# Kernel tuning notes

Hardware: AMD Instinct MI355X
Metric: run time of the kernel (lower is better)

## Reference

```python
import jax, jax.numpy as jnp
import numpy as np


def setup_inputs() -> dict:
    key = jax.random.key(0)
    ks = jax.random.split(key, 8)
    d, h = 1024, 256
    bl, bh = 2048, 2048
    b = bl + bh
    w = lambda k, shp: jax.random.normal(k, shp, jnp.float32) * 0.02
    return {
        "z_low": jax.random.normal(ks[0], (bl, d), jnp.float32),
        "z_high": jax.random.normal(ks[1], (bh, d), jnp.float32),
        "z_bar": jax.random.normal(ks[2], (b, d), jnp.float32),
        "z_normal": jax.random.normal(ks[3], (b, d), jnp.float32),
        "Wa1": w(ks[4], (d, h)), "ba1": jnp.zeros((h,), jnp.float32),
        "Wa2": w(ks[5], (h,)), "ba2": jnp.zeros((), jnp.float32),
        "W0": w(ks[6], (d, d)), "b0": jnp.zeros((d,), jnp.float32),
        "W1": w(ks[7], (d, d)), "b1": jnp.zeros((d,), jnp.float32),
    }


def _scores(x, Wa1, ba1, Wa2, ba2):
    # Linear -> tanh -> Linear(->1); returns per-row attention logits [N]
    return jnp.tanh(x @ Wa1 + ba1) @ Wa2 + ba2


def _integrate(x, Wa1, ba1, Wa2, ba2):
    a = jax.nn.softmax(_scores(x, Wa1, ba1, Wa2, ba2))  # [N]
    return a @ x  # [dim]


def _loo_pool(x, Wa1, ba1, Wa2, ba2):
    # batched leave-one-out attention pooling: row i pools over all j != i
    n = x.shape[0]
    s = _scores(x, Wa1, ba1, Wa2, ba2)  # [N]
    S = jnp.broadcast_to(s[None, :], (n, n))
    S = jnp.where(jnp.eye(n, dtype=bool), -jnp.inf, S)
    A = jax.nn.softmax(S, axis=-1)  # [N,N], zero on diagonal
    return A @ x  # [N, dim]


def _cos(a, b, eps=1e-8):
    na = jnp.maximum(jnp.linalg.norm(a, axis=-1), eps)
    nb = jnp.maximum(jnp.linalg.norm(b, axis=-1), eps)
    return jnp.sum(a * b, axis=-1) / (na * nb)


def reference(z_low, z_high, z_bar, z_normal, Wa1, ba1, Wa2, ba2, W0, b0, W1, b1):
    z_all = jnp.concatenate([z_low, z_high], axis=0)  # [B, d]
    batch = z_all.shape[0]

    z_hat = jnp.concatenate([
        _loo_pool(z_low, Wa1, ba1, Wa2, ba2),
        _loo_pool(z_high, Wa1, ba1, Wa2, ba2),
    ], axis=0)  # [B, d]
    z_tumor = _loo_pool(z_all, Wa1, ba1, Wa2, ba2)  # [B, d]
    z_norm = _integrate(z_normal, Wa1, ba1, Wa2, ba2)  # [d]

    lin0 = lambda v: v @ W0 + b0
    lin1 = lambda v: v @ W1 + b1

    base = lin0(z_hat) + lin1(z_bar)
    pred_tumor = base + lin0(z_tumor)          # [B, d]
    pred_normal = base + lin0(z_norm)[None, :]  # [B, d]

    cpc_tumor = z_all @ pred_tumor.T    # [B, B]
    cpc_normal = z_all @ pred_normal.T  # [B, B]
    eye = jnp.eye(batch, dtype=cpc_tumor.dtype)
    total = eye * cpc_tumor + (1.0 - eye) * cpc_normal

    loss_tcl = jnp.sum(jnp.diag(jax.nn.log_softmax(total, axis=1))) / (-1.0 * batch)

    ones = jnp.ones((batch,), z_all.dtype)
    cos_loss = jnp.mean(ones - _cos(z_all, z_hat)) + jnp.mean(ones - _cos(z_all, z_bar))
    hinge_in = _cos(z_all, pred_tumor) - _cos(z_all, pred_normal)
    hinge = jnp.mean(jnp.maximum(0.0, 1.0 - hinge_in))  # HingeEmbeddingLoss, target=-1, margin=1
    loss_adc = cos_loss + hinge

    return (loss_tcl, loss_adc)
```

## Files before the change

kernel.cpp:

```cpp
#include <hip/hip_runtime.h>
#include <math.h>

#define D     1024
#define H     256
#define BLOW  2048
#define BTOT  4096
#define NCHUNK 64

using bf16x8 = __attribute__((ext_vector_type(8))) __bf16;
using f32x4  = __attribute__((ext_vector_type(4))) float;

static const size_t OFF_ZALL = 0;
static const size_t OFF_C    = 4194304;
static const size_t OFF_PT   = 8388608;
static const size_t T0       = 12582912;
static const size_t OFF_SALL = T0;
static const size_t OFF_SNORM= T0 + 4096;
static const size_t OFF_EGRP = T0 + 8192;
static const size_t OFF_ENORM= T0 + 16384;
static const size_t OFF_PLOW = T0 + 20480;
static const size_t OFF_PHIGH= T0 + 21504;
static const size_t OFF_PNORM= T0 + 22528;
static const size_t OFF_PALL = T0 + 23552;
static const size_t OFF_ZNV  = T0 + 24576;
static const size_t OFF_WNORM= T0 + 25600;
static const size_t OFF_BIASC= T0 + 26624;
static const size_t OFF_STATS= T0 + 27648;
static const size_t OFF_ACC  = T0 + 27664;
static const size_t OFF_NZ   = T0 + 27680;
static const size_t OFF_DT   = T0 + 31776;
static const size_t OFF_G    = T0 + 35872;
static const size_t OFF_DIAG = T0 + 39968;
static const size_t OFF_PART = T0 + 44064;
static const size_t BF_BASE_F = 13160448;
static const size_t BF_ZALLN= 0;
static const size_t BF_ZHAT = 8388608;
static const size_t BF_ZTUM = 12582912;
static const size_t BF_ZBAR = 16777216;
static const size_t BF_C    = 20971520;
static const size_t BF_W0T  = 25165824;
static const size_t BF_W1T  = 26214400;
static const size_t BF_WA1T = 27262976;

__device__ inline unsigned short f2bf(float f){
  unsigned u = __float_as_uint(f);
  u += 0x7fffu + ((u >> 16) & 1u);
  return (unsigned short)(u >> 16);
}
__device__ inline float wave_sum(float v){
#pragma unroll
  for (int o = 32; o > 0; o >>= 1) v += __shfl_xor(v, o);
  return v;
}
__device__ inline float wave_maxf(float v){
#pragma unroll
  for (int o = 32; o > 0; o >>= 1) v = fmaxf(v, __shfl_xor(v, o));
  return v;
}
__device__ inline float block_sum(float v, float* sb){
  v = wave_sum(v);
  __syncthreads();
  if ((threadIdx.x & 63) == 0) sb[threadIdx.x >> 6] = v;
  __syncthreads();
  return sb[0] + sb[1] + sb[2] + sb[3];
}
__device__ inline float block_maxf(float v, float* sb){
  v = wave_maxf(v);
  __syncthreads();
  if ((threadIdx.x & 63) == 0) sb[threadIdx.x >> 6] = v;
  __syncthreads();
  return fmaxf(fmaxf(sb[0], sb[1]), fmaxf(sb[2], sb[3]));
}

__device__ inline void gload16(const unsigned short* g, unsigned short* l){
  __builtin_amdgcn_global_load_lds(
      (const __attribute__((address_space(1))) unsigned int*)g,
      (__attribute__((address_space(3))) unsigned int*)l, 16, 0, 0);
}

__global__ __launch_bounds__(256) void k_prep(const float* __restrict__ zl,
        const float* __restrict__ zh, const float* __restrict__ znorm,
        const float* __restrict__ zbar, float* __restrict__ za,
        unsigned short* __restrict__ zalln_bf, unsigned short* __restrict__ zbar_bf){
  int row = blockIdx.x, t = threadIdx.x, job = blockIdx.z;
  if (job == 0){
    const float4* src = (const float4*)((row < BLOW) ? (zl + (size_t)row * D)
                                                     : (zh + (size_t)(row - BLOW) * D));
    float4 v = src[t];
    ((float4*)(za + (size_t)row * D))[t] = v;
    *(ushort4*)(zalln_bf + (size_t)row * D + t * 4) =
        make_ushort4(f2bf(v.x), f2bf(v.y), f2bf(v.z), f2bf(v.w));
  } else if (job == 1){
    float4 v = ((const float4*)(znorm + (size_t)row * D))[t];
    *(ushort4*)(zalln_bf + (size_t)(BTOT + row) * D + t * 4) =
        make_ushort4(f2bf(v.x), f2bf(v.y), f2bf(v.z), f2bf(v.w));
  } else {
    float4 v = ((const float4*)(zbar + (size_t)row * D))[t];
    *(ushort4*)(zbar_bf + (size_t)row * D + t * 4) =
        make_ushort4(f2bf(v.x), f2bf(v.y), f2bf(v.z), f2bf(v.w));
  }
}

__global__ __launch_bounds__(256) void k_tconv3(const float* __restrict__ W0,
        const float* __restrict__ W1, const float* __restrict__ Wa1,
        unsigned short* __restrict__ W0T, unsigned short* __restrict__ W1T,
        unsigned short* __restrict__ Wa1T){
  __shared__ float tile[32][33];
  int z = blockIdx.z;
  const float* in; unsigned short* out; int R, C;
  if (z == 0){ in = W0; out = W0T; R = D; C = D; }
  else if (z == 1){ in = W1; out = W1T; R = D; C = D; }
  else { if (blockIdx.x >= 8) return; in = Wa1; out = Wa1T; R = D; C = H; }
  int t = threadIdx.x;
  int lr = t >> 3;
  int lc = (t & 7) << 2;
  int gr = blockIdx.y * 32, gc = blockIdx.x * 32;
  float4 v = *(const float4*)(in + (size_t)(gr + lr) * C + gc + lc);
  tile[lr][lc + 0] = v.x; tile[lr][lc + 1] = v.y; tile[lr][lc + 2] = v.z; tile[lr][lc + 3] = v.w;
  __syncthreads();
  ushort4 o = make_ushort4(f2bf(tile[lc + 0][lr]), f2bf(tile[lc + 1][lr]),
                           f2bf(tile[lc + 2][lr]), f2bf(tile[lc + 3][lr]));
  *(ushort4*)(out + (size_t)(gc + lr) * R + gr + lc) = o;
}

__global__ __launch_bounds__(256) void k_zero13(float* __restrict__ ws){
  int i = blockIdx.x * 256 + threadIdx.x;
  if (i < 8192) ws[OFF_SALL + i] = 0.f;
  else if (i < 12288) ws[OFF_PLOW + i - 8192] = 0.f;
  else if (i < 13312) ws[OFF_WNORM + i - 12288] = 0.f;
  else if (i < 13328) ws[OFF_ACC + i - 13312] = 0.f;
}

__device__ inline void mfma_core_db(const unsigned short* __restrict__ A,
                                    const unsigned short* __restrict__ B,
                                    int row0, int col0,
                                    unsigned short* lds,
                                    f32x4 acc[4][4]){
  int t = threadIdx.x;
  int l = t & 63, w = t >> 6;
  int wrow = w >> 1, wcol = w & 1;
  int g = l >> 4, c15 = l & 15;
  const unsigned short* a0 = A + (size_t)(row0 + (t >> 2)) * 1024 + ((t & 3) << 3);
  const unsigned short* a1 = a0 + (size_t)64 * 1024;
  const unsigned short* b0 = B + (size_t)(col0 + (t >> 2)) * 1024 + ((t & 3) << 3);
  const unsigned short* b1 = b0 + (size_t)64 * 1024;
  int sd = w * 512;
  int abase = (wrow * 64 + c15) * 32 + g * 8;
  int bbase = 4096 + (wcol * 64 + c15) * 32 + g * 8;
  unsigned short* buf = lds;
  unsigned short* nxt = lds + 8192;
  gload16(a0, buf + sd);
  gload16(a1, buf + 2048 + sd);
  gload16(b0, buf + 4096 + sd);
  gload16(b1, buf + 6144 + sd);
  __syncthreads();
  for (int kb = 0; kb < 1024; kb += 32){
    if (kb + 32 < 1024){
      gload16(a0 + kb + 32, nxt + sd);
      gload16(a1 + kb + 32, nxt + 2048 + sd);
      gload16(b0 + kb + 32, nxt + 4096 + sd);
      gload16(b1 + kb + 32, nxt + 6144 + sd);
    }
    bf16x8 af[4], bfr[4];
#pragma unroll
    for (int m = 0; m < 4; ++m) af[m]  = *(const bf16x8*)&buf[abase + m * 512];
#pragma unroll
    for (int n = 0; n < 4; ++n) bfr[n] = *(const bf16x8*)&buf[bbase + n * 512];
#pragma unroll
    for (int m = 0; m < 4; ++m)
#pragma unroll
      for (int n = 0; n < 4; ++n)
        acc[m][n] = __builtin_amdgcn_mfma_f32_16x16x32_bf16(af[m], bfr[n], acc[m][n], 0, 0, 0);
    __syncthreads();
    unsigned short* tmp = buf; buf = nxt; nxt = tmp;
  }
}

__global__ __launch_bounds__(256) void k_scores_bf(const unsigned short* __restrict__ Zbf,
        const unsigned short* __restrict__ Wa1T, const float* __restrict__ ba1,
        const float* __restrict__ Wa2, float* __restrict__ S){
  __shared__ __align__(16) unsigned short smem[16384];
  f32x4 acc[4][4];
  f32x4 zz = {0.f, 0.f, 0.f, 0.f};
#pragma unroll
  for (int m = 0; m < 4; ++m)
#pragma unroll
    for (int n = 0; n < 4; ++n) acc[m][n] = zz;
  int row0 = blockIdx.y * 128, col0 = blockIdx.x * 128;
  mfma_core_db(Zbf, Wa1T, row0, col0, smem, acc);
  int t = threadIdx.x, l = t & 63, w = t >> 6, wrow = w >> 1, wcol = w & 1;
  int g = l >> 4, c15 = l & 15;
#pragma unroll
  for (int m = 0; m < 4; ++m){
#pragma unroll
    for (int r = 0; r < 4; ++r){
      float v = 0.f;
#pragma unroll
      for (int n = 0; n < 4; ++n){
        int col = col0 + wcol * 64 + n * 16 + c15;
        float x = acc[m][n][r] + ba1[col];
        float e = __expf(2.f * x);
        v += (1.f - 2.f / (e + 1.f)) * Wa2[col];
      }
      v += __shfl_xor(v, 1); v += __shfl_xor(v, 2); v += __shfl_xor(v, 4); v += __shfl_xor(v, 8);
      if (c15 == 0) atomicAdd(&S[row0 + wrow * 64 + m * 16 + 4 * g + r], v);
    }
  }
}

__global__ __launch_bounds__(256) void k_gemm_cpt(const unsigned short* __restrict__ Zhat,
        const unsigned short* __restrict__ Zbar, const unsigned short* __restrict__ Ztum,
        const unsigned short* __restrict__ W0T, const unsigned short* __restrict__ W1T,
        const float* __restrict__ biasC, float* __restrict__ C,
        unsigned short* __restrict__ Cbf, float* __restrict__ PT){
  __shared__ __align__(16) unsigned short smem[16384];
  f32x4 acc[4][4];
  f32x4 zz = {0.f, 0.f, 0.f, 0.f};
#pragma unroll
  for (int m = 0; m < 4; ++m)
#pragma unroll
    for (int n = 0; n < 4; ++n) acc[m][n] = zz;
  int row0 = blockIdx.y * 128, col0 = blockIdx.x * 128;
  mfma_core_db(Zhat, W0T, row0, col0, smem, acc);
  mfma_core_db(Zbar, W1T, row0, col0, smem, acc);
  int t = threadIdx.x, l = t & 63, w = t >> 6, wrow = w >> 1, wcol = w & 1;
  int g = l >> 4, c15 = l & 15;
#pragma unroll
  for (int m = 0; m < 4; ++m){
    int row = row0 + wrow * 64 + m * 16 + 4 * g;
#pragma unroll
    for (int n = 0; n < 4; ++n){
      int col = col0 + wcol * 64 + n * 16 + c15;
      float bv = biasC[col];
#pragma unroll
      for (int r = 0; r < 4; ++r){
        float v = acc[m][n][r] + bv;
        size_t idx = (size_t)(row + r) * 1024 + col;
        C[idx] = v;
        Cbf[idx] = f2bf(v);
      }
    }
  }
  mfma_core_db(Ztum, W0T, row0, col0, smem, acc);
#pragma unroll
  for (int m = 0; m < 4; ++m){
    int row = row0 + wrow * 64 + m * 16 + 4 * g;
#pragma unroll
    for (int n = 0; n < 4; ++n){
      int col = col0 + wcol * 64 + n * 16 + c15;
      float bv = biasC[col];
#pragma unroll
      for (int r = 0; r < 4; ++r){
        size_t idx = (size_t)(row + r) * 1024 + col;
        PT[idx] = acc[m][n][r] + bv;
      }
    }
  }
}

__global__ __launch_bounds__(256) void k_gemm_lse(const unsigned short* __restrict__ A,
        const unsigned short* __restrict__ B, float2* __restrict__ partials,
        float* __restrict__ diagM){
  __shared__ __align__(16) unsigned short smem[16384];
  f32x4 acc[4][4];
  f32x4 zz = {0.f, 0.f, 0.f, 0.f};
#pragma unroll
  for (int m = 0; m < 4; ++m)
#pragma unroll
    for (int n = 0; n < 4; ++n) acc[m][n] = zz;
  int row0 = blockIdx.y * 128, col0 = blockIdx.x * 128;
  mfma_core_db(A, B, row0, col0, smem, acc);
  int t = threadIdx.x, l = t & 63, w = t >> 6, wrow = w >> 1, wcol = w & 1;
  int g = l >> 4, c15 = l & 15;
  int chunk = blockIdx.x * 2 + wcol;
#pragma unroll
  for (int m = 0; m < 4; ++m){
#pragma unroll
    for (int r = 0; r < 4; ++r){
      float lm = acc[m][0][r];
#pragma unroll
      for (int n = 1; n < 4; ++n) lm = fmaxf(lm, acc[m][n][r]);
      lm = fmaxf(lm, __shfl_xor(lm, 1));
      lm = fmaxf(lm, __shfl_xor(lm, 2));
      lm = fmaxf(lm, __shfl_xor(lm, 4));
      lm = fmaxf(lm, __shfl_xor(lm, 8));
      float ls = 0.f;
#pragma unroll
      for (int n = 0; n < 4; ++n) ls += __expf(acc[m][n][r] - lm);
      ls += __shfl_xor(ls, 1); ls += __shfl_xor(ls, 2); ls += __shfl_xor(ls, 4); ls += __shfl_xor(ls, 8);
      if (c15 == 0)
        partials[(size_t)chunk * BTOT + (row0 + wrow * 64 + m * 16 + 4 * g + r)] = make_float2(lm, ls);
    }
  }
  if (blockIdx.x == blockIdx.y && wrow == wcol && ((c15 >> 2) == g)){
#pragma unroll
    for (int m = 0; m < 4; ++m)
      diagM[row0 + wrow * 64 + m * 16 + c15] = acc[m][m][c15 & 3];
  }
}

__global__ __launch_bounds__(256) void k_stats(const float* __restrict__ s_all,
        const float* __restrict__ s_norm, float* __restrict__ e_grp,
        float* __restrict__ e_norm, float* __restrict__ stats){
  __shared__ float sb[4];
  int t = threadIdx.x;
  float va[16], vn[16];
#pragma unroll
  for (int j = 0; j < 16; ++j) va[j] = s_all[t + 256 * j];
#pragma unroll
  for (int j = 0; j < 16; ++j) vn[j] = s_norm[t + 256 * j];
  float m = -1e30f;
#pragma unroll
  for (int j = 0; j < 8; ++j) m = fmaxf(m, va[j]);
  float ml = block_maxf(m, sb);
  m = -1e30f;
#pragma unroll
  for (int j = 8; j < 16; ++j) m = fmaxf(m, va[j]);
  float mh = block_maxf(m, sb);
  m = -1e30f;
#pragma unroll
  for (int j = 0; j < 16; ++j) m = fmaxf(m, vn[j]);
  float mn = block_maxf(m, sb);
  float ma = fmaxf(ml, mh);
  float a = 0.f;
#pragma unroll
  for (int j = 0; j < 8; ++j){ float e = __expf(va[j] - ml); e_grp[t + 256 * j] = e; a += e; }
  float tl = block_sum(a, sb);
  a = 0.f;
#pragma unroll
  for (int j = 8; j < 16; ++j){ float e = __expf(va[j] - mh); e_grp[t + 256 * j] = e; a += e; }
  float th = block_sum(a, sb);
  a = 0.f;
#pragma unroll
  for (int j = 0; j < 16; ++j){ float e = __expf(vn[j] - mn); e_norm[t + 256 * j] = e; a += e; }
  float tn = block_sum(a, sb);
  if (t == 0){
    float sl = __expf(ml - ma), sh = __expf(mh - ma);
    stats[0] = ml; stats[1] = tl; stats[2] = mh; stats[3] = th;
    stats[4] = ma; stats[5] = tl * sl + th * sh; stats[6] = mn; stats[7] = tn;
    stats[8] = sl; stats[9] = sh;
  }
}

__global__ __launch_bounds__(256) void k_pvec(const float* __restrict__ z_all,
        const float* __restrict__ z_normal, const float* __restrict__ e_grp,
        const float* __restrict__ e_norm, float* __restrict__ P){
  int gz = blockIdx.z;
  const float* X; const float* E; float* Pg; int nr;
  if (gz == 0){ X = z_all;                         E = e_grp;        Pg = P;        nr = BLOW; }
  else if (gz == 1){ X = z_all + (size_t)BLOW * D; E = e_grp + BLOW; Pg = P + 1024; nr = BLOW; }
  else { X = z_normal;                             E = e_norm;       Pg = P + 2048; nr = BTOT; }
  int r0 = blockIdx.y * 16;
  if (r0 >= nr) return;
  int c4 = threadIdx.x * 4;
  float4 a = make_float4(0.f, 0.f, 0.f, 0.f);
#pragma unroll 4
  for (int r = r0; r < r0 + 16; ++r){
    float e = E[r];
    float4 x = *(const float4*)(X + (size_t)r * D + c4);
    a.x = fmaf(e, x.x, a.x); a.y = fmaf(e, x.y, a.y);
    a.z = fmaf(e, x.z, a.z); a.w = fmaf(e, x.w, a.w);
  }
  atomicAdd(&Pg[c4 + 0], a.x);
  atomicAdd(&Pg[c4 + 1], a.y);
  atomicAdd(&Pg[c4 + 2], a.z);
  atomicAdd(&Pg[c4 + 3], a.w);
}

__global__ __launch_bounds__(256) void k_smallvec(const float* __restrict__ P,
        const float* __restrict__ stats, const float* __restrict__ b0,
        const float* __restrict__ b1, float* __restrict__ P_all,
        float* __restrict__ znv, float* __restrict__ biasC){
  int c = blockIdx.x * 256 + threadIdx.x;
  znv[c] = P[2048 + c] / stats[7];
  biasC[c] = 2.f * b0[c] + b1[c];
  P_all[c] = stats[8] * P[c] + stats[9] * P[1024 + c];
}

__global__ __launch_bounds__(256) void k_wnorm(const float* __restrict__ znv,
        const float* __restrict__ W0, float* __restrict__ w_norm){
  int col = blockIdx.x * 256 + threadIdx.x;
  int kc = blockIdx.y;
  float a = 0.f;
  for (int k = kc * 128; k < kc * 128 + 128; ++k)
    a = fmaf(znv[k], W0[(size_t)k * D + col], a);
  atomicAdd(&w_norm[col], a);
}

__global__ __launch_bounds__(256) void k_zhat(const float* __restrict__ z_all,
        const float* __restrict__ z_bar, const float* __restrict__ e_grp,
        const float* __restrict__ stats,
        const float* __restrict__ P_low, const float* __restrict__ P_high,
        const float* __restrict__ P_all, unsigned short* __restrict__ zhat_bf,
        unsigned short* __restrict__ ztum_bf, float* __restrict__ nz_arr,
        float* __restrict__ accum){
  __shared__ float sb[4];
  int i = blockIdx.x, t = threadIdx.x;
  const float* Pg = (i < BLOW) ? P_low : P_high;
  float Tg = (i < BLOW) ? stats[1] : stats[3];
  float Ta = stats[5];
  float eg = e_grp[i];
  float ea = eg * ((i < BLOW) ? stats[8] : stats[9]);
  float ig = 1.f / (Tg - eg), ia = 1.f / (Ta - ea);
  size_t base = (size_t)i * D;
  float4 x  = ((const float4*)(z_all + base))[t];
  float4 pg = ((const float4*)Pg)[t];
  float4 pa = ((const float4*)P_all)[t];
  float4 zb = ((const float4*)(z_bar + base))[t];
  float4 zh, zt;
  zh.x = (pg.x - eg * x.x) * ig; zh.y = (pg.y - eg * x.y) * ig;
  zh.z = (pg.z - eg * x.z) * ig; zh.w = (pg.w - eg * x.w) * ig;
  zt.x = (pa.x - ea * x.x) * ia; zt.y = (pa.y - ea * x.y) * ia;
  zt.z = (pa.z - ea * x.z) * ia; zt.w = (pa.w - ea * x.w) * ia;
  *(ushort4*)(zhat_bf + base + t * 4) = make_ushort4(f2bf(zh.x), f2bf(zh.y), f2bf(zh.z), f2bf(zh.w));
  *(ushort4*)(ztum_bf + base + t * 4) = make_ushort4(f2bf(zt.x), f2bf(zt.y), f2bf(zt.z), f2bf(zt.w));
  float nz2 = x.x*x.x + x.y*x.y + x.z*x.z + x.w*x.w;
  float nh2 = zh.x*zh.x + zh.y*zh.y + zh.z*zh.z + zh.w*zh.w;
  float dzh = x.x*zh.x + x.y*zh.y + x.z*zh.z + x.w*zh.w;
  float nb2 = zb.x*zb.x + zb.y*zb.y + zb.z*zb.z + zb.w*zb.w;
  float dzb = x.x*zb.x + x.y*zb.y + x.z*zb.z + x.w*zb.w;
  float s_nz2 = block_sum(nz2, sb);
  float s_nh2 = block_sum(nh2, sb);
  float s_dzh = block_sum(dzh, sb);
  float s_nb2 = block_sum(nb2, sb);
  float s_dzb = block_sum(dzb, sb);
  if (t == 0){
    float nz = sqrtf(s_nz2);
    nz_arr[i] = nz;
    float denA = fmaxf(nz, 1e-8f) * fmaxf(sqrtf(s_nh2), 1e-8f);
    float denB = fmaxf(nz, 1e-8f) * fmaxf(sqrtf(s_nb2), 1e-8f);
    atomicAdd(&accum[0], (1.f - s_dzh / denA) + (1.f - s_dzb / denB));
  }
}

__global__ __launch_bounds__(256) void k_rowred2(const float* __restrict__ z_all,
        const float* __restrict__ PT, const float* __restrict__ C,
        const float* __restrict__ w_norm, const float* __restrict__ nz_arr,
        float* __restrict__ dt_arr, float* __restrict__ g_arr, float* __restrict__ accum){
  __shared__ float sb[4];
  int i = blockIdx.x, t = threadIdx.x;
  size_t base = (size_t)i * D;
  float4 x  = ((const float4*)(z_all + base))[t];
  float4 pt = ((const float4*)(PT + base))[t];
  float4 c  = ((const float4*)(C + base))[t];
  float4 wv = ((const float4*)w_norm)[t];
  float4 pn = make_float4(c.x + wv.x, c.y + wv.y, c.z + wv.z, c.w + wv.w);
  float dt   = x.x*pt.x + x.y*pt.y + x.z*pt.z + x.w*pt.w;
  float npt2 = pt.x*pt.x + pt.y*pt.y + pt.z*pt.z + pt.w*pt.w;
  float dpn  = x.x*pn.x + x.y*pn.y + x.z*pn.z + x.w*pn.w;
  float npn2 = pn.x*pn.x + pn.y*pn.y + pn.z*pn.z + pn.w*pn.w;
  float gg   = x.x*wv.x + x.y*wv.y + x.z*wv.z + x.w*wv.w;
  float s_dt   = block_sum(dt, sb);
  float s_npt2 = block_sum(npt2, sb);
  float s_dpn  = block_sum(dpn, sb);
  float s_npn2 = block_sum(npn2, sb);
  float s_g    = block_sum(gg, sb);
  if (t == 0){
    dt_arr[i] = s_dt; g_arr[i] = s_g;
    float nz = fmaxf(nz_arr[i], 1e-8f);
    float ct = s_dt  / (nz * fmaxf(sqrtf(s_npt2), 1e-8f));
    float cn = s_dpn / (nz * fmaxf(sqrtf(s_npn2), 1e-8f));
    atomicAdd(&accum[1], fmaxf(0.f, 1.f - (ct - cn)));
  }
}

__global__ __launch_bounds__(256) void k_combine(const float2* __restrict__ partials,
        const float* __restrict__ diagM, const float* __restrict__ dt,
        const float* __restrict__ g, float* __restrict__ accum){
  __shared__ float sb[4];
  int i = blockIdx.x * 256 + threadIdx.x;
  float m = -1e30f, S = 0.f;
  for (int c = 0; c < NCHUNK; ++c){
    float2 p = partials[(size_t)c * BTOT + i];
    float nm = fmaxf(m, p.x);
    S = S * __expf(m - nm) + p.y * __expf(p.x - nm);
    m = nm;
  }
  float vold = diagM[i];
  float vnew = dt[i] - g[i];
  float nm = fmaxf(m, vnew);
  float S2 = S * __expf(m - nm) - __expf(vold - nm) + __expf(vnew - nm);
  float lse = g[i] + nm + logf(S2);
  float contrib = lse - dt[i];
  float tot = block_sum(contrib, sb);
  if (threadIdx.x == 0) atomicAdd(&accum[2], tot);
}

__global__ void k_final(const float* __restrict__ accum, float* __restrict__ out){
  out[0] = accum[2] / (float)BTOT;
  out[1] = (accum[0] + accum[1]) / (float)BTOT;
}

extern "C" void kernel_launch(void* const* d_in, const int* in_sizes, int n_in,
                              void* d_out, int out_size, void* d_ws, size_t ws_size,
                              hipStream_t stream){
  const float* z_low    = (const float*)d_in[0];
  const float* z_high   = (const float*)d_in[1];
  const float* z_bar    = (const float*)d_in[2];
  const float* z_normal = (const float*)d_in[3];
  const float* Wa1      = (const float*)d_in[4];
  const float* ba1      = (const float*)d_in[5];
  const float* Wa2      = (const float*)d_in[6];
  const float* ba2      = (const float*)d_in[7];
  const float* W0       = (const float*)d_in[8];
  const float* b0       = (const float*)d_in[9];
  const float* W1       = (const float*)d_in[10];
  const float* b1       = (const float*)d_in[11];
  float* ws = (float*)d_ws;
  unsigned short* bw = (unsigned short*)(ws + BF_BASE_F);
  float* out = (float*)d_out;
  (void)ba2;

  k_prep<<<dim3(BTOT, 1, 3), dim3(256), 0, stream>>>(z_low, z_high, z_normal, z_bar,
      ws + OFF_ZALL, bw + BF_ZALLN, bw + BF_ZBAR);
  k_tconv3<<<dim3(32, 32, 3), dim3(256), 0, stream>>>(W0, W1, Wa1,
      bw + BF_W0T, bw + BF_W1T, bw + BF_WA1T);
  k_zero13<<<dim3(53), dim3(256), 0, stream>>>(ws);

  k_scores_bf<<<dim3(2, 64), dim3(256), 0, stream>>>(bw + BF_ZALLN, bw + BF_WA1T,
      ba1, Wa2, ws + OFF_SALL);

  k_stats<<<dim3(1), dim3(256), 0, stream>>>(ws + OFF_SALL, ws + OFF_SNORM,
      ws + OFF_EGRP, ws + OFF_ENORM, ws + OFF_STATS);

  k_pvec<<<dim3(1, 256, 3), dim3(256), 0, stream>>>(ws + OFF_ZALL, z_normal,
      ws + OFF_EGRP, ws + OFF_ENORM, ws + OFF_PLOW);

  k_smallvec<<<dim3(4), dim3(256), 0, stream>>>(ws + OFF_PLOW, ws + OFF_STATS,
      b0, b1, ws + OFF_PALL, ws + OFF_ZNV, ws + OFF_BIASC);

  k_wnorm<<<dim3(4, 8), dim3(256), 0, stream>>>(ws + OFF_ZNV, W0, ws + OFF_WNORM);

  k_zhat<<<dim3(BTOT), dim3(256), 0, stream>>>(ws + OFF_ZALL, z_bar,
      ws + OFF_EGRP, ws + OFF_STATS,
      ws + OFF_PLOW, ws + OFF_PHIGH, ws + OFF_PALL,
      bw + BF_ZHAT, bw + BF_ZTUM, ws + OFF_NZ, ws + OFF_ACC);

  k_gemm_cpt<<<dim3(8, 32), dim3(256), 0, stream>>>(bw + BF_ZHAT, bw + BF_ZBAR,
      bw + BF_ZTUM, bw + BF_W0T, bw + BF_W1T, ws + OFF_BIASC,
      ws + OFF_C, bw + BF_C, ws + OFF_PT);

  k_rowred2<<<dim3(BTOT), dim3(256), 0, stream>>>(ws + OFF_ZALL, ws + OFF_PT,
      ws + OFF_C, ws + OFF_WNORM, ws + OFF_NZ, ws + OFF_DT, ws + OFF_G, ws + OFF_ACC);

  k_gemm_lse<<<dim3(32, 32), dim3(256), 0, stream>>>(bw + BF_ZALLN, bw + BF_C,
      (float2*)(ws + OFF_PART), ws + OFF_DIAG);

  k_combine<<<dim3(16), dim3(256), 0, stream>>>((const float2*)(ws + OFF_PART),
      ws + OFF_DIAG, ws + OFF_DT, ws + OFF_G, ws + OFF_ACC);

  k_final<<<dim3(1), dim3(1), 0, stream>>>(ws + OFF_ACC, out);
}
```

Baseline: 409.3 us.

## Split tumor GEMM into separate z-slice and enlarge LSE GEMM tile to 256 rows

The C/PT GEMM kernel now launches a second z-slice of blocks, so the Ztum·W0 product runs in parallel with the Zhat·W0+Zbar·W1 product rather than after it in the same block. It writes only the raw Ztum·W0 product (D2), and the row-reduction kernel adds C back to rebuild pred_tumor. Separately, the LSE GEMM now uses 256x128 tiles with an 8x4 accumulator per wave and a larger LDS buffer, which halves the grid and increases reuse of the B tile. The larger tile raises register and LDS use, which may lower occupancy, and the diagonal extraction now uses a per-element compare loop.

```diff
diff --git a/kernel.cpp b/kernel.cpp
--- a/kernel.cpp
+++ b/kernel.cpp
@@ -12,7 +12,7 @@
 
 static const size_t OFF_ZALL = 0;
 static const size_t OFF_C    = 4194304;
-static const size_t OFF_PT   = 8388608;
+static const size_t OFF_D2   = 8388608;
 static const size_t T0       = 12582912;
 static const size_t OFF_SALL = T0;
 static const size_t OFF_SNORM= T0 + 4096;
@@ -176,6 +176,59 @@
   }
 }
 
+__device__ inline void mfma_core256(const unsigned short* __restrict__ A,
+                                    const unsigned short* __restrict__ B,
+                                    int row0, int col0,
+                                    unsigned short* lds,
+                                    f32x4 acc[8][4]){
+  int t = threadIdx.x;
+  int l = t & 63, w = t >> 6;
+  int wr = w >> 1, wc = w & 1;
+  int g = l >> 4, c15 = l & 15;
+  const unsigned short* aP[4];
+  const unsigned short* bP[2];
+#pragma unroll
+  for (int j = 0; j < 4; ++j){
+    int c = t + 256 * j;
+    aP[j] = A + (size_t)(row0 + (c >> 2)) * 1024 + ((c & 3) << 3);
+  }
+#pragma unroll
+  for (int j = 0; j < 2; ++j){
+    int c = t + 256 * j;
+    bP[j] = B + (size_t)(col0 + (c >> 2)) * 1024 + ((c & 3) << 3);
+  }
+  int sd = w * 512;
+  int abase = (wr * 128 + c15) * 32 + g * 8;
+  int bbase = 8192 + (wc * 64 + c15) * 32 + g * 8;
+  unsigned short* buf = lds;
+  unsigned short* nxt = lds + 12288;
+#pragma unroll
+  for (int j = 0; j < 4; ++j) gload16(aP[j], buf + sd + j * 2048);
+#pragma unroll
+  for (int j = 0; j < 2; ++j) gload16(bP[j], buf + 8192 + sd + j * 2048);
+  __syncthreads();
+  for (int kb = 0; kb < 1024; kb += 32){
+    if (kb + 32 < 1024){
+#pragma unroll
+      for (int j = 0; j < 4; ++j) gload16(aP[j] + kb + 32, nxt + sd + j * 2048);
+#pragma unroll
+      for (int j = 0; j < 2; ++j) gload16(bP[j] + kb + 32, nxt + 8192 + sd + j * 2048);
+    }
+    bf16x8 bfr[4];
+#pragma unroll
+    for (int n = 0; n < 4; ++n) bfr[n] = *(const bf16x8*)&buf[bbase + n * 512];
+#pragma unroll
+    for (int m = 0; m < 8; ++m){
+      bf16x8 af = *(const bf16x8*)&buf[abase + m * 512];
+#pragma unroll
+      for (int n = 0; n < 4; ++n)
+        acc[m][n] = __builtin_amdgcn_mfma_f32_16x16x32_bf16(af, bfr[n], acc[m][n], 0, 0, 0);
+    }
+    __syncthreads();
+    unsigned short* tmp = buf; buf = nxt; nxt = tmp;
+  }
+}
+
 __global__ __launch_bounds__(256) void k_scores_bf(const unsigned short* __restrict__ Zbf,
         const unsigned short* __restrict__ Wa1T, const float* __restrict__ ba1,
         const float* __restrict__ Wa2, float* __restrict__ S){
@@ -212,7 +265,7 @@
         const unsigned short* __restrict__ Zbar, const unsigned short* __restrict__ Ztum,
         const unsigned short* __restrict__ W0T, const unsigned short* __restrict__ W1T,
         const float* __restrict__ biasC, float* __restrict__ C,
-        unsigned short* __restrict__ Cbf, float* __restrict__ PT){
+        unsigned short* __restrict__ Cbf, float* __restrict__ D2){
   __shared__ __align__(16) unsigned short smem[16384];
   f32x4 acc[4][4];
   f32x4 zz = {0.f, 0.f, 0.f, 0.f};
@@ -221,38 +274,38 @@
 #pragma unroll
     for (int n = 0; n < 4; ++n) acc[m][n] = zz;
   int row0 = blockIdx.y * 128, col0 = blockIdx.x * 128;
-  mfma_core_db(Zhat, W0T, row0, col0, smem, acc);
-  mfma_core_db(Zbar, W1T, row0, col0, smem, acc);
   int t = threadIdx.x, l = t & 63, w = t >> 6, wrow = w >> 1, wcol = w & 1;
   int g = l >> 4, c15 = l & 15;
-#pragma unroll
-  for (int m = 0; m < 4; ++m){
-    int row = row0 + wrow * 64 + m * 16 + 4 * g;
-#pragma unroll
-    for (int n = 0; n < 4; ++n){
-      int col = col0 + wcol * 64 + n * 16 + c15;
-      float bv = biasC[col];
-#pragma unroll
-      for (int r = 0; r < 4; ++r){
-        float v = acc[m][n][r] + bv;
-        size_t idx = (size_t)(row + r) * 1024 + col;
-        C[idx] = v;
-        Cbf[idx] = f2bf(v);
+  if (blockIdx.z == 0){
+    mfma_core_db(Zhat, W0T, row0, col0, smem, acc);
+    mfma_core_db(Zbar, W1T, row0, col0, smem, acc);
+#pragma unroll
+    for (int m = 0; m < 4; ++m){
+      int row = row0 + wrow * 64 + m * 16 + 4 * g;
+#pragma unroll
+      for (int n = 0; n < 4; ++n){
+        int col = col0 + wcol * 64 + n * 16 + c15;
+        float bv = biasC[col];
+#pragma unroll
+        for (int r = 0; r < 4; ++r){
+          float v = acc[m][n][r] + bv;
+          size_t idx = (size_t)(row + r) * 1024 + col;
+          C[idx] = v;
+          Cbf[idx] = f2bf(v);
+        }
       }
     }
-  }
-  mfma_core_db(Ztum, W0T, row0, col0, smem, acc);
-#pragma unroll
-  for (int m = 0; m < 4; ++m){
-    int row = row0 + wrow * 64 + m * 16 + 4 * g;
-#pragma unroll
-    for (int n = 0; n < 4; ++n){
-      int col = col0 + wcol * 64 + n * 16 + c15;
-      float bv = biasC[col];
-#pragma unroll
-      for (int r = 0; r < 4; ++r){
-        size_t idx = (size_t)(row + r) * 1024 + col;
-        PT[idx] = acc[m][n][r] + bv;
+  } else {
+    mfma_core_db(Ztum, W0T, row0, col0, smem, acc);
+#pragma unroll
+    for (int m = 0; m < 4; ++m){
+      int row = row0 + wrow * 64 + m * 16 + 4 * g;
+#pragma unroll
+      for (int n = 0; n < 4; ++n){
+        int col = col0 + wcol * 64 + n * 16 + c15;
+#pragma unroll
+        for (int r = 0; r < 4; ++r)
+          D2[(size_t)(row + r) * 1024 + col] = acc[m][n][r];
       }
     }
   }
@@ -261,20 +314,20 @@
 __global__ __launch_bounds__(256) void k_gemm_lse(const unsigned short* __restrict__ A,
         const unsigned short* __restrict__ B, float2* __restrict__ partials,
         float* __restrict__ diagM){
-  __shared__ __align__(16) unsigned short smem[16384];
-  f32x4 acc[4][4];
+  __shared__ __align__(16) unsigned short smem[24576];
+  f32x4 acc[8][4];
   f32x4 zz = {0.f, 0.f, 0.f, 0.f};
 #pragma unroll
-  for (int m = 0; m < 4; ++m)
+  for (int m = 0; m < 8; ++m)
 #pragma unroll
     for (int n = 0; n < 4; ++n) acc[m][n] = zz;
-  int row0 = blockIdx.y * 128, col0 = blockIdx.x * 128;
-  mfma_core_db(A, B, row0, col0, smem, acc);
-  int t = threadIdx.x, l = t & 63, w = t >> 6, wrow = w >> 1, wcol = w & 1;
+  int row0 = blockIdx.y * 256, col0 = blockIdx.x * 128;
+  mfma_core256(A, B, row0, col0, smem, acc);
+  int t = threadIdx.x, l = t & 63, w = t >> 6, wr = w >> 1, wc = w & 1;
   int g = l >> 4, c15 = l & 15;
-  int chunk = blockIdx.x * 2 + wcol;
-#pragma unroll
-  for (int m = 0; m < 4; ++m){
+  int chunk = blockIdx.x * 2 + wc;
+#pragma unroll
+  for (int m = 0; m < 8; ++m){
 #pragma unroll
     for (int r = 0; r < 4; ++r){
       float lm = acc[m][0][r];
@@ -289,13 +342,22 @@
       for (int n = 0; n < 4; ++n) ls += __expf(acc[m][n][r] - lm);
       ls += __shfl_xor(ls, 1); ls += __shfl_xor(ls, 2); ls += __shfl_xor(ls, 4); ls += __shfl_xor(ls, 8);
       if (c15 == 0)
-        partials[(size_t)chunk * BTOT + (row0 + wrow * 64 + m * 16 + 4 * g + r)] = make_float2(lm, ls);
-    }
-  }
-  if (blockIdx.x == blockIdx.y && wrow == wcol && ((c15 >> 2) == g)){
-#pragma unroll
-    for (int m = 0; m < 4; ++m)
-      diagM[row0 + wrow * 64 + m * 16 + c15] = acc[m][m][c15 & 3];
+        partials[(size_t)chunk * BTOT + (row0 + wr * 128 + m * 16 + 4 * g + r)] = make_float2(lm, ls);
+    }
+  }
+  if (col0 >= row0 && col0 < row0 + 256){
+#pragma unroll
+    for (int m = 0; m < 8; ++m){
+#pragma unroll
+      for (int n = 0; n < 4; ++n){
+        int col = col0 + wc * 64 + n * 16 + c15;
+#pragma unroll
+        for (int r = 0; r < 4; ++r){
+          int row = row0 + wr * 128 + m * 16 + 4 * g + r;
+          if (row == col) diagM[row] = acc[m][n][r];
+        }
+      }
+    }
   }
 }
 
@@ -434,16 +496,17 @@
 }
 
 __global__ __launch_bounds__(256) void k_rowred2(const float* __restrict__ z_all,
-        const float* __restrict__ PT, const float* __restrict__ C,
+        const float* __restrict__ D2, const float* __restrict__ C,
         const float* __restrict__ w_norm, const float* __restrict__ nz_arr,
         float* __restrict__ dt_arr, float* __restrict__ g_arr, float* __restrict__ accum){
   __shared__ float sb[4];
   int i = blockIdx.x, t = threadIdx.x;
   size_t base = (size_t)i * D;
   float4 x  = ((const float4*)(z_all + base))[t];
-  float4 pt = ((const float4*)(PT + base))[t];
+  float4 d2 = ((const float4*)(D2 + base))[t];
   float4 c  = ((const float4*)(C + base))[t];
   float4 wv = ((const float4*)w_norm)[t];
+  float4 pt = make_float4(c.x + d2.x, c.y + d2.y, c.z + d2.z, c.w + d2.w);
   float4 pn = make_float4(c.x + wv.x, c.y + wv.y, c.z + wv.z, c.w + wv.w);
   float dt   = x.x*pt.x + x.y*pt.y + x.z*pt.z + x.w*pt.w;
   float npt2 = pt.x*pt.x + pt.y*pt.y + pt.z*pt.z + pt.w*pt.w;
@@ -536,14 +599,14 @@
       ws + OFF_PLOW, ws + OFF_PHIGH, ws + OFF_PALL,
       bw + BF_ZHAT, bw + BF_ZTUM, ws + OFF_NZ, ws + OFF_ACC);
 
-  k_gemm_cpt<<<dim3(8, 32), dim3(256), 0, stream>>>(bw + BF_ZHAT, bw + BF_ZBAR,
+  k_gemm_cpt<<<dim3(8, 32, 2), dim3(256), 0, stream>>>(bw + BF_ZHAT, bw + BF_ZBAR,
       bw + BF_ZTUM, bw + BF_W0T, bw + BF_W1T, ws + OFF_BIASC,
-      ws + OFF_C, bw + BF_C, ws + OFF_PT);
-
-  k_rowred2<<<dim3(BTOT), dim3(256), 0, stream>>>(ws + OFF_ZALL, ws + OFF_PT,
+      ws + OFF_C, bw + BF_C, ws + OFF_D2);
+
+  k_rowred2<<<dim3(BTOT), dim3(256), 0, stream>>>(ws + OFF_ZALL, ws + OFF_D2,
       ws + OFF_C, ws + OFF_WNORM, ws + OFF_NZ, ws + OFF_DT, ws + OFF_G, ws + OFF_ACC);
 
-  k_gemm_lse<<<dim3(32, 32), dim3(256), 0, stream>>>(bw + BF_ZALLN, bw + BF_C,
+  k_gemm_lse<<<dim3(32, 16), dim3(256), 0, stream>>>(bw + BF_ZALLN, bw + BF_C,
       (float2*)(ws + OFF_PART), ws + OFF_DIAG);
 
   k_combine<<<dim3(16), dim3(256), 0, stream>>>((const float2*)(ws + OFF_PART),
```

Result: no change. 412.0 us (+0.7%).

## Split projection GEMM into concatenated-K and tumor-delta grid slices with lighter sync

Applied to the files above, without the earlier changes.

The z_hat·W0 and z_bar·W1 products now run as one K=2048 GEMM over row-concatenated bf16 inputs and weights. The z_tumor·W0 product becomes a separate grid slice along z that writes only a delta matrix, so the grid doubles and the serial triple GEMM per block goes away. PT is rebuilt in the row-reduction kernel from the bf16 C plus the delta, which drops the fp32 C and PT writes but adds bf16 rounding to C in the cosine terms. The inner GEMM loop also replaces __syncthreads with explicit vmcnt waits and raw s_barrier to overlap the next tile's loads.

```diff
diff --git a/kernel.cpp b/kernel.cpp
--- a/kernel.cpp
+++ b/kernel.cpp
@@ -11,16 +11,13 @@
 using f32x4  = __attribute__((ext_vector_type(4))) float;
 
 static const size_t OFF_ZALL = 0;
-static const size_t OFF_C    = 4194304;
-static const size_t OFF_PT   = 8388608;
-static const size_t T0       = 12582912;
+static const size_t OFF_D2   = 4194304;
+static const size_t T0       = 8388608;
 static const size_t OFF_SALL = T0;
 static const size_t OFF_SNORM= T0 + 4096;
 static const size_t OFF_EGRP = T0 + 8192;
 static const size_t OFF_ENORM= T0 + 16384;
 static const size_t OFF_PLOW = T0 + 20480;
-static const size_t OFF_PHIGH= T0 + 21504;
-static const size_t OFF_PNORM= T0 + 22528;
 static const size_t OFF_PALL = T0 + 23552;
 static const size_t OFF_ZNV  = T0 + 24576;
 static const size_t OFF_WNORM= T0 + 25600;
@@ -32,20 +29,21 @@
 static const size_t OFF_G    = T0 + 35872;
 static const size_t OFF_DIAG = T0 + 39968;
 static const size_t OFF_PART = T0 + 44064;
-static const size_t BF_BASE_F = 13160448;
+static const size_t BF_BASE_F = 8972288;
 static const size_t BF_ZALLN= 0;
-static const size_t BF_ZHAT = 8388608;
-static const size_t BF_ZTUM = 12582912;
-static const size_t BF_ZBAR = 16777216;
+static const size_t BF_ZCAT = 8388608;
+static const size_t BF_ZTUM = 16777216;
 static const size_t BF_C    = 20971520;
-static const size_t BF_W0T  = 25165824;
-static const size_t BF_W1T  = 26214400;
+static const size_t BF_WCAT = 25165824;
 static const size_t BF_WA1T = 27262976;
 
 __device__ inline unsigned short f2bf(float f){
   unsigned u = __float_as_uint(f);
   u += 0x7fffu + ((u >> 16) & 1u);
   return (unsigned short)(u >> 16);
+}
+__device__ inline float bf2f(unsigned short u){
+  return __uint_as_float(((unsigned)u) << 16);
 }
 __device__ inline float wave_sum(float v){
 #pragma unroll
@@ -81,7 +79,7 @@
 __global__ __launch_bounds__(256) void k_prep(const float* __restrict__ zl,
         const float* __restrict__ zh, const float* __restrict__ znorm,
         const float* __restrict__ zbar, float* __restrict__ za,
-        unsigned short* __restrict__ zalln_bf, unsigned short* __restrict__ zbar_bf){
+        unsigned short* __restrict__ zalln_bf, unsigned short* __restrict__ zcat_bf){
   int row = blockIdx.x, t = threadIdx.x, job = blockIdx.z;
   if (job == 0){
     const float4* src = (const float4*)((row < BLOW) ? (zl + (size_t)row * D)
@@ -96,21 +94,20 @@
         make_ushort4(f2bf(v.x), f2bf(v.y), f2bf(v.z), f2bf(v.w));
   } else {
     float4 v = ((const float4*)(zbar + (size_t)row * D))[t];
-    *(ushort4*)(zbar_bf + (size_t)row * D + t * 4) =
+    *(ushort4*)(zcat_bf + (size_t)row * 2048 + 1024 + t * 4) =
         make_ushort4(f2bf(v.x), f2bf(v.y), f2bf(v.z), f2bf(v.w));
   }
 }
 
 __global__ __launch_bounds__(256) void k_tconv3(const float* __restrict__ W0,
         const float* __restrict__ W1, const float* __restrict__ Wa1,
-        unsigned short* __restrict__ W0T, unsigned short* __restrict__ W1T,
-        unsigned short* __restrict__ Wa1T){
+        unsigned short* __restrict__ WCAT, unsigned short* __restrict__ Wa1T){
   __shared__ float tile[32][33];
   int z = blockIdx.z;
-  const float* in; unsigned short* out; int R, C;
-  if (z == 0){ in = W0; out = W0T; R = D; C = D; }
-  else if (z == 1){ in = W1; out = W1T; R = D; C = D; }
-  else { if (blockIdx.x >= 8) return; in = Wa1; out = Wa1T; R = D; C = H; }
+  const float* in; unsigned short* out; int C, ostride;
+  if (z == 0){ in = W0; out = WCAT; C = D; ostride = 2048; }
+  else if (z == 1){ in = W1; out = WCAT + 1024; C = D; ostride = 2048; }
+  else { if (blockIdx.x >= 8) return; in = Wa1; out = Wa1T; C = H; ostride = 1024; }
   int t = threadIdx.x;
   int lr = t >> 3;
   int lc = (t & 7) << 2;
@@ -120,7 +117,7 @@
   __syncthreads();
   ushort4 o = make_ushort4(f2bf(tile[lc + 0][lr]), f2bf(tile[lc + 1][lr]),
                            f2bf(tile[lc + 2][lr]), f2bf(tile[lc + 3][lr]));
-  *(ushort4*)(out + (size_t)(gc + lr) * R + gr + lc) = o;
+  *(ushort4*)(out + (size_t)(gc + lr) * ostride + gr + lc) = o;
 }
 
 __global__ __launch_bounds__(256) void k_zero13(float* __restrict__ ws){
@@ -131,19 +128,18 @@
   else if (i < 13328) ws[OFF_ACC + i - 13312] = 0.f;
 }
 
-__device__ inline void mfma_core_db(const unsigned short* __restrict__ A,
-                                    const unsigned short* __restrict__ B,
-                                    int row0, int col0,
-                                    unsigned short* lds,
-                                    f32x4 acc[4][4]){
+__device__ inline void mfma_core_cv(const unsigned short* __restrict__ A, int sA,
+                                    const unsigned short* __restrict__ B, int sB,
+                                    int K, int row0, int col0,
+                                    unsigned short* lds, f32x4 acc[4][4]){
   int t = threadIdx.x;
   int l = t & 63, w = t >> 6;
   int wrow = w >> 1, wcol = w & 1;
   int g = l >> 4, c15 = l & 15;
-  const unsigned short* a0 = A + (size_t)(row0 + (t >> 2)) * 1024 + ((t & 3) << 3);
-  const unsigned short* a1 = a0 + (size_t)64 * 1024;
-  const unsigned short* b0 = B + (size_t)(col0 + (t >> 2)) * 1024 + ((t & 3) << 3);
-  const unsigned short* b1 = b0 + (size_t)64 * 1024;
+  const unsigned short* a0 = A + (size_t)(row0 + (t >> 2)) * sA + ((t & 3) << 3);
+  const unsigned short* a1 = a0 + (size_t)64 * sA;
+  const unsigned short* b0 = B + (size_t)(col0 + (t >> 2)) * sB + ((t & 3) << 3);
+  const unsigned short* b1 = b0 + (size_t)64 * sB;
   int sd = w * 512;
   int abase = (wrow * 64 + c15) * 32 + g * 8;
   int bbase = 4096 + (wcol * 64 + c15) * 32 + g * 8;
@@ -153,14 +149,19 @@
   gload16(a1, buf + 2048 + sd);
   gload16(b0, buf + 4096 + sd);
   gload16(b1, buf + 6144 + sd);
-  __syncthreads();
-  for (int kb = 0; kb < 1024; kb += 32){
-    if (kb + 32 < 1024){
+  for (int kb = 0; kb < K; kb += 32){
+    if (kb + 32 < K){
       gload16(a0 + kb + 32, nxt + sd);
       gload16(a1 + kb + 32, nxt + 2048 + sd);
       gload16(b0 + kb + 32, nxt + 4096 + sd);
       gload16(b1 + kb + 32, nxt + 6144 + sd);
+      asm volatile("s_waitcnt vmcnt(4)" ::: "memory");
+    } else {
+      asm volatile("s_waitcnt vmcnt(0)" ::: "memory");
     }
+    __builtin_amdgcn_sched_barrier(0);
+    __builtin_amdgcn_s_barrier();
+    __builtin_amdgcn_sched_barrier(0);
     bf16x8 af[4], bfr[4];
 #pragma unroll
     for (int m = 0; m < 4; ++m) af[m]  = *(const bf16x8*)&buf[abase + m * 512];
@@ -171,7 +172,9 @@
 #pragma unroll
       for (int n = 0; n < 4; ++n)
         acc[m][n] = __builtin_amdgcn_mfma_f32_16x16x32_bf16(af[m], bfr[n], acc[m][n], 0, 0, 0);
-    __syncthreads();
+    __builtin_amdgcn_sched_barrier(0);
+    __builtin_amdgcn_s_barrier();
+    __builtin_amdgcn_sched_barrier(0);
     unsigned short* tmp = buf; buf = nxt; nxt = tmp;
   }
 }
@@ -187,7 +190,7 @@
 #pragma unroll
     for (int n = 0; n < 4; ++n) acc[m][n] = zz;
   int row0 = blockIdx.y * 128, col0 = blockIdx.x * 128;
-  mfma_core_db(Zbf, Wa1T, row0, col0, smem, acc);
+  mfma_core_cv(Zbf, 1024, Wa1T, 1024, 1024, row0, col0, smem, acc);
   int t = threadIdx.x, l = t & 63, w = t >> 6, wrow = w >> 1, wcol = w & 1;
   int g = l >> 4, c15 = l & 15;
 #pragma unroll
@@ -208,11 +211,10 @@
   }
 }
 
-__global__ __launch_bounds__(256) void k_gemm_cpt(const unsigned short* __restrict__ Zhat,
-        const unsigned short* __restrict__ Zbar, const unsigned short* __restrict__ Ztum,
-        const unsigned short* __restrict__ W0T, const unsigned short* __restrict__ W1T,
-        const float* __restrict__ biasC, float* __restrict__ C,
-        unsigned short* __restrict__ Cbf, float* __restrict__ PT){
+__global__ __launch_bounds__(256) void k_gemm_cd(const unsigned short* __restrict__ ZCAT,
+        const unsigned short* __restrict__ ZTUM, const unsigned short* __restrict__ WCAT,
+        const float* __restrict__ biasC, unsigned short* __restrict__ Cbf,
+        float* __restrict__ D2){
   __shared__ __align__(16) unsigned short smem[16384];
   f32x4 acc[4][4];
   f32x4 zz = {0.f, 0.f, 0.f, 0.f};
@@ -221,38 +223,33 @@
 #pragma unroll
     for (int n = 0; n < 4; ++n) acc[m][n] = zz;
   int row0 = blockIdx.y * 128, col0 = blockIdx.x * 128;
-  mfma_core_db(Zhat, W0T, row0, col0, smem, acc);
-  mfma_core_db(Zbar, W1T, row0, col0, smem, acc);
   int t = threadIdx.x, l = t & 63, w = t >> 6, wrow = w >> 1, wcol = w & 1;
   int g = l >> 4, c15 = l & 15;
-#pragma unroll
-  for (int m = 0; m < 4; ++m){
-    int row = row0 + wrow * 64 + m * 16 + 4 * g;
-#pragma unroll
-    for (int n = 0; n < 4; ++n){
-      int col = col0 + wcol * 64 + n * 16 + c15;
-      float bv = biasC[col];
-#pragma unroll
-      for (int r = 0; r < 4; ++r){
-        float v = acc[m][n][r] + bv;
-        size_t idx = (size_t)(row + r) * 1024 + col;
-        C[idx] = v;
-        Cbf[idx] = f2bf(v);
+  if (blockIdx.z == 0){
+    mfma_core_cv(ZCAT, 2048, WCAT, 2048, 2048, row0, col0, smem, acc);
+#pragma unroll
+    for (int m = 0; m < 4; ++m){
+      int row = row0 + wrow * 64 + m * 16 + 4 * g;
+#pragma unroll
+      for (int n = 0; n < 4; ++n){
+        int col = col0 + wcol * 64 + n * 16 + c15;
+        float bv = biasC[col];
+#pragma unroll
+        for (int r = 0; r < 4; ++r)
+          Cbf[(size_t)(row + r) * 1024 + col] = f2bf(acc[m][n][r] + bv);
       }
     }
-  }
-  mfma_core_db(Ztum, W0T, row0, col0, smem, acc);
-#pragma unroll
-  for (int m = 0; m < 4; ++m){
-    int row = row0 + wrow * 64 + m * 16 + 4 * g;
-#pragma unroll
-    for (int n = 0; n < 4; ++n){
-      int col = col0 + wcol * 64 + n * 16 + c15;
-      float bv = biasC[col];
-#pragma unroll
-      for (int r = 0; r < 4; ++r){
-        size_t idx = (size_t)(row + r) * 1024 + col;
-        PT[idx] = acc[m][n][r] + bv;
+  } else {
+    mfma_core_cv(ZTUM, 1024, WCAT, 2048, 1024, row0, col0, smem, acc);
+#pragma unroll
+    for (int m = 0; m < 4; ++m){
+      int row = row0 + wrow * 64 + m * 16 + 4 * g;
+#pragma unroll
+      for (int n = 0; n < 4; ++n){
+        int col = col0 + wcol * 64 + n * 16 + c15;
+#pragma unroll
+        for (int r = 0; r < 4; ++r)
+          D2[(size_t)(row + r) * 1024 + col] = acc[m][n][r];
       }
     }
   }
@@ -269,7 +266,7 @@
 #pragma unroll
     for (int n = 0; n < 4; ++n) acc[m][n] = zz;
   int row0 = blockIdx.y * 128, col0 = blockIdx.x * 128;
-  mfma_core_db(A, B, row0, col0, smem, acc);
+  mfma_core_cv(A, 1024, B, 1024, 1024, row0, col0, smem, acc);
   int t = threadIdx.x, l = t & 63, w = t >> 6, wrow = w >> 1, wcol = w & 1;
   int g = l >> 4, c15 = l & 15;
   int chunk = blockIdx.x * 2 + wcol;
@@ -391,7 +388,7 @@
         const float* __restrict__ z_bar, const float* __restrict__ e_grp,
         const float* __restrict__ stats,
         const float* __restrict__ P_low, const float* __restrict__ P_high,
-        const float* __restrict__ P_all, unsigned short* __restrict__ zhat_bf,
+        const float* __restrict__ P_all, unsigned short* __restrict__ zcat_bf,
         unsigned short* __restrict__ ztum_bf, float* __restrict__ nz_arr,
         float* __restrict__ accum){
   __shared__ float sb[4];
@@ -412,7 +409,8 @@
   zh.z = (pg.z - eg * x.z) * ig; zh.w = (pg.w - eg * x.w) * ig;
   zt.x = (pa.x - ea * x.x) * ia; zt.y = (pa.y - ea * x.y) * ia;
   zt.z = (pa.z - ea * x.z) * ia; zt.w = (pa.w - ea * x.w) * ia;
-  *(ushort4*)(zhat_bf + base + t * 4) = make_ushort4(f2bf(zh.x), f2bf(zh.y), f2bf(zh.z), f2bf(zh.w));
+  *(ushort4*)(zcat_bf + (size_t)i * 2048 + t * 4) =
+      make_ushort4(f2bf(zh.x), f2bf(zh.y), f2bf(zh.z), f2bf(zh.w));
   *(ushort4*)(ztum_bf + base + t * 4) = make_ushort4(f2bf(zt.x), f2bf(zt.y), f2bf(zt.z), f2bf(zt.w));
   float nz2 = x.x*x.x + x.y*x.y + x.z*x.z + x.w*x.w;
   float nh2 = zh.x*zh.x + zh.y*zh.y + zh.z*zh.z + zh.w*zh.w;
@@ -434,16 +432,18 @@
 }
 
 __global__ __launch_bounds__(256) void k_rowred2(const float* __restrict__ z_all,
-        const float* __restrict__ PT, const float* __restrict__ C,
+        const float* __restrict__ D2, const unsigned short* __restrict__ Cbf,
         const float* __restrict__ w_norm, const float* __restrict__ nz_arr,
         float* __restrict__ dt_arr, float* __restrict__ g_arr, float* __restrict__ accum){
   __shared__ float sb[4];
   int i = blockIdx.x, t = threadIdx.x;
   size_t base = (size_t)i * D;
   float4 x  = ((const float4*)(z_all + base))[t];
-  float4 pt = ((const float4*)(PT + base))[t];
-  float4 c  = ((const float4*)(C + base))[t];
+  float4 d2 = ((const float4*)(D2 + base))[t];
+  ushort4 cu = *(const ushort4*)(Cbf + base + t * 4);
+  float4 c = make_float4(bf2f(cu.x), bf2f(cu.y), bf2f(cu.z), bf2f(cu.w));
   float4 wv = ((const float4*)w_norm)[t];
+  float4 pt = make_float4(c.x + d2.x, c.y + d2.y, c.z + d2.z, c.w + d2.w);
   float4 pn = make_float4(c.x + wv.x, c.y + wv.y, c.z + wv.z, c.w + wv.w);
   float dt   = x.x*pt.x + x.y*pt.y + x.z*pt.z + x.w*pt.w;
   float npt2 = pt.x*pt.x + pt.y*pt.y + pt.z*pt.z + pt.w*pt.w;
@@ -512,9 +512,9 @@
   (void)ba2;
 
   k_prep<<<dim3(BTOT, 1, 3), dim3(256), 0, stream>>>(z_low, z_high, z_normal, z_bar,
-      ws + OFF_ZALL, bw + BF_ZALLN, bw + BF_ZBAR);
+      ws + OFF_ZALL, bw + BF_ZALLN, bw + BF_ZCAT);
   k_tconv3<<<dim3(32, 32, 3), dim3(256), 0, stream>>>(W0, W1, Wa1,
-      bw + BF_W0T, bw + BF_W1T, bw + BF_WA1T);
+      bw + BF_WCAT, bw + BF_WA1T);
   k_zero13<<<dim3(53), dim3(256), 0, stream>>>(ws);
 
   k_scores_bf<<<dim3(2, 64), dim3(256), 0, stream>>>(bw + BF_ZALLN, bw + BF_WA1T,
@@ -533,15 +533,14 @@
 
   k_zhat<<<dim3(BTOT), dim3(256), 0, stream>>>(ws + OFF_ZALL, z_bar,
       ws + OFF_EGRP, ws + OFF_STATS,
-      ws + OFF_PLOW, ws + OFF_PHIGH, ws + OFF_PALL,
-      bw + BF_ZHAT, bw + BF_ZTUM, ws + OFF_NZ, ws + OFF_ACC);
-
-  k_gemm_cpt<<<dim3(8, 32), dim3(256), 0, stream>>>(bw + BF_ZHAT, bw + BF_ZBAR,
-      bw + BF_ZTUM, bw + BF_W0T, bw + BF_W1T, ws + OFF_BIASC,
-      ws + OFF_C, bw + BF_C, ws + OFF_PT);
-
-  k_rowred2<<<dim3(BTOT), dim3(256), 0, stream>>>(ws + OFF_ZALL, ws + OFF_PT,
-      ws + OFF_C, ws + OFF_WNORM, ws + OFF_NZ, ws + OFF_DT, ws + OFF_G, ws + OFF_ACC);
+      ws + OFF_PLOW, ws + OFF_PLOW + 1024, ws + OFF_PALL,
+      bw + BF_ZCAT, bw + BF_ZTUM, ws + OFF_NZ, ws + OFF_ACC);
+
+  k_gemm_cd<<<dim3(8, 32, 2), dim3(256), 0, stream>>>(bw + BF_ZCAT, bw + BF_ZTUM,
+      bw + BF_WCAT, ws + OFF_BIASC, bw + BF_C, ws + OFF_D2);
+
+  k_rowred2<<<dim3(BTOT), dim3(256), 0, stream>>>(ws + OFF_ZALL, ws + OFF_D2,
+      bw + BF_C, ws + OFF_WNORM, ws + OFF_NZ, ws + OFF_DT, ws + OFF_G, ws + OFF_ACC);
 
   k_gemm_lse<<<dim3(32, 32), dim3(256), 0, stream>>>(bw + BF_ZALLN, bw + BF_C,
       (float2*)(ws + OFF_PART), ws + OFF_DIAG);
```

Result: faster. 388.1 us (-5.2%).
